# Performance work log

Measured on AMD Instinct MI355X. Metric: run time of the kernel, lower is better.

Reference implementation:

```python
import jax, jax.numpy as jnp
import numpy as np

EPS = 1e-8
THR = 1e-6


def setup_inputs() -> dict:
    key = jax.random.key(0)
    ks = jax.random.split(key, 16)
    B, N, E, F, H, NH = 2, 8192, 131072, 128, 256, 4
    D = H // NH          # per-head width = 64
    FEAT = 2 * F + 12    # 268 = 2F + radial + dist + dot + 9 so3
    s = 0.05
    return {
        "h": jax.random.normal(ks[0], (B, N, F), jnp.float32),
        "coord": jax.random.normal(ks[1], (B, N, 3), jnp.float32),
        "edge_index": jax.random.randint(ks[2], (2, E), 0, N),
        "edge_w1": jax.random.normal(ks[3], (NH, FEAT, D), jnp.float32) * s,
        "edge_b1": jnp.zeros((NH, D), jnp.float32),
        "edge_w2": jax.random.normal(ks[4], (NH, D, D), jnp.float32) * s,
        "edge_b2": jnp.zeros((NH, D), jnp.float32),
        "ln_g": jnp.ones((H,), jnp.float32),
        "ln_b": jnp.zeros((H,), jnp.float32),
        "node_w1": jax.random.normal(ks[5], (H + F, H), jnp.float32) * s,
        "node_b1": jnp.zeros((H,), jnp.float32),
        "node_w2": jax.random.normal(ks[6], (H, F), jnp.float32) * s,
        "node_b2": jnp.zeros((F,), jnp.float32),
        "coord_w1": jax.random.normal(ks[7], (H, H), jnp.float32) * s,
        "coord_b1": jnp.zeros((H,), jnp.float32),
        "coord_w2": jax.random.normal(ks[8], (H, 1), jnp.float32) * 0.001,  # xavier gain 0.001
    }


def reference(h, coord, edge_index, edge_w1, edge_b1, edge_w2, edge_b2,
              ln_g, ln_b, node_w1, node_b1, node_w2, node_b2,
              coord_w1, coord_b1, coord_w2):
    B, N, F = h.shape
    row, col = edge_index[0], edge_index[1]
    ci, ck = coord[:, row], coord[:, col]            # (B,E,3) gathers
    coord_diff = ci - ck
    radial = jnp.sum(coord_diff * coord_diff, axis=-1, keepdims=True)
    dist = jnp.sqrt(radial)
    dot = jnp.sum(ci * ck, axis=-1, keepdims=True)
    # SO3 local frame per edge
    a = coord_diff / (dist + EPS)
    cr = jnp.cross(ci, ck)
    b = cr / (jnp.linalg.norm(cr, axis=-1, keepdims=True) + EPS)
    c = jnp.cross(a, b)
    bad = ((jnp.linalg.norm(a, axis=-1) < THR) |
           (jnp.linalg.norm(b, axis=-1) < THR) |
           (jnp.linalg.norm(c, axis=-1) < THR))
    so3 = jnp.stack([a, b, c], axis=-1)              # (B,E,3,3) columns a,b,c
    eye = jnp.broadcast_to(jnp.eye(3, dtype=so3.dtype), so3.shape)
    so3 = jnp.where(bad[..., None, None], eye, so3).reshape(B, -1, 9)
    # edge features -> multi-head edge MLPs
    feat = jnp.concatenate([h[:, row], h[:, col], radial, dist, dot, so3], axis=-1)  # (B,E,268)
    hmid = jax.nn.silu(jnp.einsum('bef,hfd->bhed', feat, edge_w1) + edge_b1[None, :, None, :])
    heads = jnp.einsum('bhed,hdk->bhek', hmid, edge_w2) + edge_b2[None, :, None, :]
    combined = jnp.moveaxis(heads, 1, 2).reshape(B, heads.shape[2], -1)  # (B,E,H)
    mu = jnp.mean(combined, axis=-1, keepdims=True)
    var = jnp.var(combined, axis=-1, keepdims=True)
    edge_feat = (combined - mu) / jnp.sqrt(var + 1e-5) * ln_g + ln_b
    # coordinate update: scatter-add weighted coord_diff
    w = jax.nn.silu(edge_feat @ coord_w1 + coord_b1) @ coord_w2   # (B,E,1)
    seg = lambda d: jax.ops.segment_sum(d, row, num_segments=N)
    coord_out = coord + jax.vmap(seg)(coord_diff * w)
    # node update: scatter-add edge features then MLP with residual
    agg = jax.vmap(seg)(edge_feat)                                # (B,N,H)
    out = jnp.concatenate([h, agg], axis=-1)
    out = jax.nn.silu(out @ node_w1 + node_b1) @ node_w2 + node_b2
    return h + out, coord_out
```

## Files before the change

### kernel.cpp

```cpp
#include <hip/hip_runtime.h>
#include <hip/hip_bf16.h>
#include <cstdint>
#include <cstddef>

#define BB 2
#define NN 8192
#define EE 131072
#define FFdim 128
#define HHdim 256
#define NHEAD 4
#define DHEAD 64
#define FEATD 268
#define K1PAD 288
#define SF 296
#define SH 264
#define TE 64
#define NT 32
#define SA 392
#define SM 264

typedef short bf16x8 __attribute__((ext_vector_type(8)));
typedef float floatx4 __attribute__((ext_vector_type(4)));

__device__ __forceinline__ float silu_f(float x) {
    return x * __fdividef(1.0f, 1.0f + __expf(-x));
}
__device__ __forceinline__ unsigned short f2bf(float x) {
    unsigned int u = __float_as_uint(x);
    unsigned int r = (u + 0x7fffu + ((u >> 16) & 1u)) >> 16;
    return (unsigned short)r;
}
__device__ __forceinline__ float bf2f(unsigned short u) {
    return __uint_as_float(((unsigned int)u) << 16);
}
__device__ __forceinline__ unsigned int pk2bf(float x, float y) {
    float2 f = { x, y };
    __hip_bfloat162 t = __float22bfloat162_rn(f);
    union { __hip_bfloat162 b; unsigned int u; } cv;
    cv.b = t;
    return cv.u;
}
__device__ __forceinline__ float rowsum16(float v) {
    v += __int_as_float(__builtin_amdgcn_update_dpp(0, __float_as_int(v), 0x128, 0xf, 0xf, true));
    v += __int_as_float(__builtin_amdgcn_update_dpp(0, __float_as_int(v), 0x124, 0xf, 0xf, true));
    v += __int_as_float(__builtin_amdgcn_update_dpp(0, __float_as_int(v), 0x122, 0xf, 0xf, true));
    v += __int_as_float(__builtin_amdgcn_update_dpp(0, __float_as_int(v), 0x121, 0xf, 0xf, true));
    return v;
}
__device__ __forceinline__ int operm(int p) { return ((p & 3) << 4) | (p >> 2); }

#define W1T_ELEMS (256 * K1PAD)
#define W2T_ELEMS (256 * 64)
#define CW1T_ELEMS (256 * 256)
#define NW1T_ELEMS (256 * 384)
#define NW2T_ELEMS (128 * 256)
#define HBF_ELEMS (BB * NN * FFdim)
#define WT_A (W1T_ELEMS)
#define WT_B (W1T_ELEMS + W2T_ELEMS)
#define WT_C (W1T_ELEMS + W2T_ELEMS + CW1T_ELEMS)
#define WT_D (WT_C + NW1T_ELEMS)
#define WT_E (WT_D + NW2T_ELEMS)
#define WT_F (WT_E + NN)
#define WT_G (WT_F + HBF_ELEMS)
__global__ void prep_weights(const float* __restrict__ w1,
                             const float* __restrict__ w2,
                             const float* __restrict__ cw1,
                             const float* __restrict__ nw1,
                             const float* __restrict__ nw2,
                             const float* __restrict__ h,
                             unsigned short* __restrict__ w1T,
                             unsigned short* __restrict__ w2T,
                             unsigned short* __restrict__ cw1T,
                             unsigned short* __restrict__ nw1T,
                             unsigned short* __restrict__ nw2T,
                             unsigned short* __restrict__ hbf,
                             int* __restrict__ counts) {
    int idx = blockIdx.x * blockDim.x + threadIdx.x;
    if (idx < WT_A) {
        int n = idx / K1PAD, k = idx % K1PAD;
        int hh = n >> 6, d = n & 63;
        float v = (k < FEATD) ? w1[((size_t)hh * FEATD + k) * DHEAD + d] : 0.f;
        w1T[idx] = f2bf(v);
    } else if (idx < WT_B) {
        int j = idx - WT_A;
        int n = j >> 6, p = j & 63;
        int hh = n >> 6, dout = n & 63;
        int din = operm(p);
        w2T[j] = f2bf(w2[(size_t)hh * 4096 + din * 64 + dout]);
    } else if (idx < WT_C) {
        int j = idx - WT_B;
        int n = j >> 8, P = j & 255;
        int ko = (P >> 6) * 64 + operm(P & 63);
        cw1T[j] = f2bf(cw1[ko * 256 + n]);
    } else if (idx < WT_D) {
        int j = idx - WT_C;
        int n = j / 384, k = j % 384;
        int ko = (k < 128) ? k : 128 + ((k - 128) >> 6) * 64 + operm(k & 63);
        nw1T[j] = f2bf(nw1[ko * 256 + n]);
    } else if (idx < WT_E) {
        int j = idx - WT_D;
        int n = j >> 8, P = j & 255;
        int ko = (P >> 6) * 64 + operm(P & 63);
        nw2T[j] = f2bf(nw2[ko * 128 + n]);
    } else if (idx < WT_F) {
        counts[idx - WT_E] = 0;
    } else if (idx < WT_G) {
        int j = idx - WT_F;
        hbf[j] = f2bf(h[j]);
    }
}

__global__ void csr_count(const int* __restrict__ eidx, int* __restrict__ counts) {
    int e = blockIdx.x * 256 + threadIdx.x;
    atomicAdd(&counts[eidx[e]], 1);
}

__global__ void csr_scan(const int* __restrict__ counts,
                         int* __restrict__ offsets,
                         int* __restrict__ cursor) {
    __shared__ int wsum[4];
    const int t = threadIdx.x;
    const int base = t * 32;
    int local[32];
    int s = 0;
#pragma unroll
    for (int i = 0; i < 32; ++i) { local[i] = counts[base + i]; s += local[i]; }
    const int lane = t & 63, w = t >> 6;
    int v = s;
#pragma unroll
    for (int off = 1; off < 64; off <<= 1) {
        int u = __shfl_up(v, off, 64);
        if (lane >= off) v += u;
    }
    if (lane == 63) wsum[w] = v;
    __syncthreads();
    int wbase = 0;
    for (int i = 0; i < w; ++i) wbase += wsum[i];
    int run = wbase + v - s;
#pragma unroll
    for (int i = 0; i < 32; ++i) {
        offsets[base + i] = run;
        cursor[base + i] = run;
        run += local[i];
    }
    if (t == 255) offsets[NN] = run;
}

__global__ void csr_fill(const int* __restrict__ eidx,
                         int* __restrict__ cursor, int* __restrict__ perm) {
    int e = blockIdx.x * 256 + threadIdx.x;
    int r = eidx[e];
    int pos = atomicAdd(&cursor[r], 1);
    perm[e] = pos;
}

__global__ __launch_bounds__(256, 4)
void edge_kernel(const unsigned short* __restrict__ hbf,
                 const float* __restrict__ coord,
                 const int* __restrict__ eidx,
                 const int* __restrict__ perm,
                 const unsigned short* __restrict__ w1T, const float* __restrict__ b1,
                 const unsigned short* __restrict__ w2T, const float* __restrict__ b2,
                 const float* __restrict__ lng, const float* __restrict__ lnb,
                 const unsigned short* __restrict__ cw1T, const float* __restrict__ cb1,
                 const float* __restrict__ cw2,
                 unsigned short* __restrict__ efb, float4* __restrict__ wd) {
    __shared__ unsigned short bufA[TE * SF];
    __shared__ int slot_s[TE];
    __shared__ float cd_s[TE][3];
    __shared__ float lns[TE], lns2[TE];
    __shared__ float scr[TE * 4];

    const int tid = threadIdx.x;
    const int b = blockIdx.y;
    const int e0 = blockIdx.x * TE;
    const int lane = tid & 63;
    const int w = tid >> 6;
    const int lm = lane & 15;
    const int quad = lane >> 4;
    const int koff = quad * 8;

    if (tid < TE) {
        lns[tid] = 0.f; lns2[tid] = 0.f;
        const int e = e0 + tid;
        const int r = eidx[e], c = eidx[EE + e];
        slot_s[tid] = perm[e];
        const float* pi = coord + ((size_t)b * NN + r) * 3;
        const float* pk = coord + ((size_t)b * NN + c) * 3;
        float ci0 = pi[0], ci1 = pi[1], ci2 = pi[2];
        float ck0 = pk[0], ck1 = pk[1], ck2 = pk[2];
        float dx = ci0 - ck0, dy = ci1 - ck1, dz = ci2 - ck2;
        float radial = dx * dx + dy * dy + dz * dz;
        float dist = sqrtf(radial);
        float dotv = ci0 * ck0 + ci1 * ck1 + ci2 * ck2;
        float inva = __fdividef(1.0f, dist + 1e-8f);
        float a0 = dx * inva, a1 = dy * inva, a2 = dz * inva;
        float cr0 = ci1 * ck2 - ci2 * ck1;
        float cr1 = ci2 * ck0 - ci0 * ck2;
        float cr2 = ci0 * ck1 - ci1 * ck0;
        float nb = sqrtf(cr0 * cr0 + cr1 * cr1 + cr2 * cr2);
        float invb = __fdividef(1.0f, nb + 1e-8f);
        float b0 = cr0 * invb, b1v = cr1 * invb, b2v = cr2 * invb;
        float c0 = a1 * b2v - a2 * b1v;
        float c1 = a2 * b0 - a0 * b2v;
        float c2 = a0 * b1v - a1 * b0;
        float na = sqrtf(a0 * a0 + a1 * a1 + a2 * a2);
        float nbn = sqrtf(b0 * b0 + b1v * b1v + b2v * b2v);
        float nc = sqrtf(c0 * c0 + c1 * c1 + c2 * c2);
        bool bad = (na < 1e-6f) || (nbn < 1e-6f) || (nc < 1e-6f);
        float s[12];
        s[0] = radial; s[1] = dist; s[2] = dotv;
        if (bad) {
            s[3] = 1.f; s[4] = 0.f; s[5] = 0.f;
            s[6] = 0.f; s[7] = 1.f; s[8] = 0.f;
            s[9] = 0.f; s[10] = 0.f; s[11] = 1.f;
        } else {
            s[3] = a0;  s[4] = b0;  s[5] = c0;
            s[6] = a1;  s[7] = b1v; s[8] = c1;
            s[9] = a2;  s[10] = b2v; s[11] = c2;
        }
        unsigned short* fp = &bufA[tid * SF];
#pragma unroll
        for (int q = 0; q < 12; ++q) fp[256 + q] = f2bf(s[q]);
#pragma unroll
        for (int q = FEATD; q < K1PAD; ++q) fp[q] = 0;
        cd_s[tid][0] = dx; cd_s[tid][1] = dy; cd_s[tid][2] = dz;
    }
    for (int idx = tid; idx < TE * 32; idx += 256) {
        const int e = idx >> 5, c16 = idx & 31;
        const int node = (c16 < 16) ? eidx[e0 + e] : eidx[EE + e0 + e];
        const int cc = (c16 & 15) * 8;
        uint4 v = *(const uint4*)&hbf[((size_t)b * NN + node) * FFdim + cc];
        *(uint4*)&bufA[e * SF + c16 * 8] = v;
    }
    __syncthreads();

    floatx4 acc[4][4];
#pragma unroll
    for (int i = 0; i < 4; ++i)
#pragma unroll
        for (int j = 0; j < 4; ++j)
#pragma unroll
            for (int q = 0; q < 4; ++q) acc[i][j][q] = 0.f;
#pragma unroll
    for (int ks = 0; ks < K1PAD / 32; ++ks) {
        const int kb = ks * 32 + koff;
        bf16x8 a[4], bfr[4];
#pragma unroll
        for (int rt = 0; rt < 4; ++rt)
            a[rt] = *(const bf16x8*)&bufA[(rt * 16 + lm) * SF + kb];
#pragma unroll
        for (int ct = 0; ct < 4; ++ct)
            bfr[ct] = *(const bf16x8*)&w1T[(size_t)(w * 64 + ct * 16 + lm) * K1PAD + kb];
#pragma unroll
        for (int rt = 0; rt < 4; ++rt)
#pragma unroll
            for (int ct = 0; ct < 4; ++ct)
                acc[rt][ct] = __builtin_amdgcn_mfma_f32_16x16x32_bf16(
                    a[rt], bfr[ct], acc[rt][ct], 0, 0, 0);
    }
    float bias1[4];
#pragma unroll
    for (int ct = 0; ct < 4; ++ct) bias1[ct] = b1[w * 64 + ct * 16 + lm];
    __syncthreads();
#pragma unroll
    for (int rt = 0; rt < 4; ++rt)
#pragma unroll
        for (int reg = 0; reg < 4; ++reg) {
            const int row = rt * 16 + quad * 4 + reg;
            uint2 pk;
            pk.x = pk2bf(silu_f(acc[rt][0][reg] + bias1[0]),
                         silu_f(acc[rt][1][reg] + bias1[1]));
            pk.y = pk2bf(silu_f(acc[rt][2][reg] + bias1[2]),
                         silu_f(acc[rt][3][reg] + bias1[3]));
            *(uint2*)&bufA[row * SH + w * 64 + lm * 4] = pk;
        }

    floatx4 acc2[4][4];
#pragma unroll
    for (int i = 0; i < 4; ++i)
#pragma unroll
        for (int j = 0; j < 4; ++j)
#pragma unroll
            for (int q = 0; q < 4; ++q) acc2[i][j][q] = 0.f;
#pragma unroll
    for (int ks = 0; ks < 2; ++ks) {
        const int kb = ks * 32 + koff;
        bf16x8 a[4], bfr[4];
#pragma unroll
        for (int rt = 0; rt < 4; ++rt)
            a[rt] = *(const bf16x8*)&bufA[(rt * 16 + lm) * SH + w * 64 + kb];
#pragma unroll
        for (int ct = 0; ct < 4; ++ct)
            bfr[ct] = *(const bf16x8*)&w2T[(size_t)(w * 64 + ct * 16 + lm) * 64 + kb];
#pragma unroll
        for (int rt = 0; rt < 4; ++rt)
#pragma unroll
            for (int ct = 0; ct < 4; ++ct)
                acc2[rt][ct] = __builtin_amdgcn_mfma_f32_16x16x32_bf16(
                    a[rt], bfr[ct], acc2[rt][ct], 0, 0, 0);
    }
    float bias2[4];
#pragma unroll
    for (int ct = 0; ct < 4; ++ct) bias2[ct] = b2[w * 64 + ct * 16 + lm];
#pragma unroll
    for (int rt = 0; rt < 4; ++rt)
#pragma unroll
        for (int reg = 0; reg < 4; ++reg) {
            float s = 0.f, s2 = 0.f;
#pragma unroll
            for (int ct = 0; ct < 4; ++ct) {
                float v = acc2[rt][ct][reg] + bias2[ct];
                acc2[rt][ct][reg] = v;
                s += v; s2 += v * v;
            }
            s = rowsum16(s);
            s2 = rowsum16(s2);
            if (lm == 0) {
                const int row = rt * 16 + quad * 4 + reg;
                atomicAdd(&lns[row], s);
                atomicAdd(&lns2[row], s2);
            }
        }
    __syncthreads();
    if (tid < TE) {
        float mean = lns[tid] * (1.0f / 256.0f);
        float var = lns2[tid] * (1.0f / 256.0f) - mean * mean;
        scr[tid] = mean;
        scr[TE + tid] = rsqrtf(var + 1e-5f);
    }
    __syncthreads();
    {
        float gv[4], bv[4];
#pragma unroll
        for (int ct = 0; ct < 4; ++ct) {
            const int col = w * 64 + ct * 16 + lm;
            gv[ct] = lng[col]; bv[ct] = lnb[col];
        }
#pragma unroll
        for (int rt = 0; rt < 4; ++rt)
#pragma unroll
            for (int reg = 0; reg < 4; ++reg) {
                const int row = rt * 16 + quad * 4 + reg;
                const float mu = scr[row], rs = scr[TE + row];
                uint2 pk;
                pk.x = pk2bf((acc2[rt][0][reg] - mu) * rs * gv[0] + bv[0],
                             (acc2[rt][1][reg] - mu) * rs * gv[1] + bv[1]);
                pk.y = pk2bf((acc2[rt][2][reg] - mu) * rs * gv[2] + bv[2],
                             (acc2[rt][3][reg] - mu) * rs * gv[3] + bv[3]);
                *(uint2*)&bufA[row * SH + w * 64 + lm * 4] = pk;
            }
    }
    __syncthreads();

    floatx4 acc3[4][4];
#pragma unroll
    for (int i = 0; i < 4; ++i)
#pragma unroll
        for (int j = 0; j < 4; ++j)
#pragma unroll
            for (int q = 0; q < 4; ++q) acc3[i][j][q] = 0.f;
#pragma unroll
    for (int ks = 0; ks < 8; ++ks) {
        const int kb = ks * 32 + koff;
        bf16x8 a[4], bfr[4];
#pragma unroll
        for (int rt = 0; rt < 4; ++rt)
            a[rt] = *(const bf16x8*)&bufA[(rt * 16 + lm) * SH + kb];
#pragma unroll
        for (int ct = 0; ct < 4; ++ct)
            bfr[ct] = *(const bf16x8*)&cw1T[(size_t)(w * 64 + ct * 16 + lm) * 256 + kb];
#pragma unroll
        for (int rt = 0; rt < 4; ++rt)
#pragma unroll
            for (int ct = 0; ct < 4; ++ct)
                acc3[rt][ct] = __builtin_amdgcn_mfma_f32_16x16x32_bf16(
                    a[rt], bfr[ct], acc3[rt][ct], 0, 0, 0);
    }
    {
        float cb[4], cwv[4];
#pragma unroll
        for (int ct = 0; ct < 4; ++ct) {
            const int col = w * 64 + ct * 16 + lm;
            cb[ct] = cb1[col]; cwv[ct] = cw2[col];
        }
#pragma unroll
        for (int rt = 0; rt < 4; ++rt)
#pragma unroll
            for (int reg = 0; reg < 4; ++reg) {
                float s = 0.f;
#pragma unroll
                for (int ct = 0; ct < 4; ++ct)
                    s += silu_f(acc3[rt][ct][reg] + cb[ct]) * cwv[ct];
                s = rowsum16(s);
                if (lm == 0) scr[(rt * 16 + quad * 4 + reg) * 4 + w] = s;
            }
    }
    __syncthreads();

    if (tid < TE) {
        float ww = scr[tid * 4] + scr[tid * 4 + 1] + scr[tid * 4 + 2] + scr[tid * 4 + 3];
        float4 o = { cd_s[tid][0] * ww, cd_s[tid][1] * ww, cd_s[tid][2] * ww, 0.f };
        wd[(size_t)b * EE + slot_s[tid]] = o;
    }
    for (int idx = tid; idx < TE * 32; idx += 256) {
        const int e = idx >> 5, c = idx & 31;
        uint4 v = *(const uint4*)&bufA[e * SH + c * 8];
        *(uint4*)&efb[((size_t)b * EE + slot_s[e]) * HHdim + c * 8] = v;
    }
}

__global__ __launch_bounds__(256, 4)
void node_kernel(const float* __restrict__ h,
                 const unsigned short* __restrict__ hbf,
                 const float* __restrict__ coord,
                 const unsigned short* __restrict__ efb,
                 const float4* __restrict__ wd,
                 const int* __restrict__ offsets,
                 const unsigned short* __restrict__ nw1T, const float* __restrict__ nb1,
                 const unsigned short* __restrict__ nw2T, const float* __restrict__ nb2,
                 float* __restrict__ hout, float* __restrict__ coord_out) {
    __shared__ unsigned short bufN[NT * SA];

    const int tid = threadIdx.x;
    const int b = blockIdx.y;
    const int n0 = blockIdx.x * NT;
    const int lane = tid & 63;
    const int w = tid >> 6;
    const int lm = lane & 15;
    const int quad = lane >> 4;
    const int koff = quad * 8;

    for (int idx = tid; idx < NT * 16; idx += 256) {
        const int r = idx >> 4, c8 = idx & 15;
        uint4 v = *(const uint4*)&hbf[((size_t)b * NN + n0 + r) * FFdim + c8 * 8];
        *(uint4*)&bufN[r * SA + c8 * 8] = v;
    }

    for (int i = 0; i < 8; ++i) {
        const int r = w * 8 + i;
        const int n = n0 + r;
        const int o0 = offsets[n], o1 = offsets[n + 1];
        float a0 = 0.f, a1 = 0.f, a2 = 0.f, a3 = 0.f;
        const unsigned short* ebase = efb + (size_t)b * EE * HHdim + lane * 4;
        int j = o0;
        for (; j + 4 <= o1; j += 4) {
            ushort4 u0 = *(const ushort4*)(ebase + (size_t)(j + 0) * HHdim);
            ushort4 u1 = *(const ushort4*)(ebase + (size_t)(j + 1) * HHdim);
            ushort4 u2 = *(const ushort4*)(ebase + (size_t)(j + 2) * HHdim);
            ushort4 u3 = *(const ushort4*)(ebase + (size_t)(j + 3) * HHdim);
            a0 += bf2f(u0.x) + bf2f(u1.x) + bf2f(u2.x) + bf2f(u3.x);
            a1 += bf2f(u0.y) + bf2f(u1.y) + bf2f(u2.y) + bf2f(u3.y);
            a2 += bf2f(u0.z) + bf2f(u1.z) + bf2f(u2.z) + bf2f(u3.z);
            a3 += bf2f(u0.w) + bf2f(u1.w) + bf2f(u2.w) + bf2f(u3.w);
        }
        for (; j < o1; ++j) {
            ushort4 u = *(const ushort4*)(ebase + (size_t)j * HHdim);
            a0 += bf2f(u.x); a1 += bf2f(u.y); a2 += bf2f(u.z); a3 += bf2f(u.w);
        }
        uint2 pk;
        pk.x = pk2bf(a0, a1);
        pk.y = pk2bf(a2, a3);
        *(uint2*)&bufN[r * SA + FFdim + lane * 4] = pk;

        float sx = 0.f, sy = 0.f, sz = 0.f;
        for (int jj = o0 + lane; jj < o1; jj += 64) {
            float4 t = wd[(size_t)b * EE + jj];
            sx += t.x; sy += t.y; sz += t.z;
        }
#pragma unroll
        for (int m = 1; m < 64; m <<= 1) {
            sx += __shfl_xor(sx, m, 64);
            sy += __shfl_xor(sy, m, 64);
            sz += __shfl_xor(sz, m, 64);
        }
        if (lane < 3) {
            const size_t cb = ((size_t)b * NN + n) * 3 + lane;
            float s = (lane == 0) ? sx : (lane == 1) ? sy : sz;
            coord_out[cb] = coord[cb] + s;
        }
    }
    __syncthreads();

    floatx4 acc[2][4];
#pragma unroll
    for (int i = 0; i < 2; ++i)
#pragma unroll
        for (int j = 0; j < 4; ++j)
#pragma unroll
            for (int q = 0; q < 4; ++q) acc[i][j][q] = 0.f;
#pragma unroll
    for (int ks = 0; ks < 12; ++ks) {
        const int kb = ks * 32 + koff;
        bf16x8 a[2], bfr[4];
#pragma unroll
        for (int rt = 0; rt < 2; ++rt)
            a[rt] = *(const bf16x8*)&bufN[(rt * 16 + lm) * SA + kb];
#pragma unroll
        for (int ct = 0; ct < 4; ++ct)
            bfr[ct] = *(const bf16x8*)&nw1T[(size_t)(w * 64 + ct * 16 + lm) * 384 + kb];
#pragma unroll
        for (int rt = 0; rt < 2; ++rt)
#pragma unroll
            for (int ct = 0; ct < 4; ++ct)
                acc[rt][ct] = __builtin_amdgcn_mfma_f32_16x16x32_bf16(
                    a[rt], bfr[ct], acc[rt][ct], 0, 0, 0);
    }
    float nb1v[4];
#pragma unroll
    for (int ct = 0; ct < 4; ++ct) nb1v[ct] = nb1[w * 64 + ct * 16 + lm];
    __syncthreads();
#pragma unroll
    for (int rt = 0; rt < 2; ++rt)
#pragma unroll
        for (int reg = 0; reg < 4; ++reg) {
            const int row = rt * 16 + quad * 4 + reg;
            uint2 pk;
            pk.x = pk2bf(silu_f(acc[rt][0][reg] + nb1v[0]),
                         silu_f(acc[rt][1][reg] + nb1v[1]));
            pk.y = pk2bf(silu_f(acc[rt][2][reg] + nb1v[2]),
                         silu_f(acc[rt][3][reg] + nb1v[3]));
            *(uint2*)&bufN[row * SM + w * 64 + lm * 4] = pk;
        }
    __syncthreads();

    floatx4 accb[2][2];
#pragma unroll
    for (int i = 0; i < 2; ++i)
#pragma unroll
        for (int j = 0; j < 2; ++j)
#pragma unroll
            for (int q = 0; q < 4; ++q) accb[i][j][q] = 0.f;
#pragma unroll
    for (int ks = 0; ks < 8; ++ks) {
        const int kb = ks * 32 + koff;
        bf16x8 a[2], bfr[2];
#pragma unroll
        for (int rt = 0; rt < 2; ++rt)
            a[rt] = *(const bf16x8*)&bufN[(rt * 16 + lm) * SM + kb];
#pragma unroll
        for (int ct = 0; ct < 2; ++ct)
            bfr[ct] = *(const bf16x8*)&nw2T[(size_t)(w * 32 + ct * 16 + lm) * 256 + kb];
#pragma unroll
        for (int rt = 0; rt < 2; ++rt)
#pragma unroll
            for (int ct = 0; ct < 2; ++ct)
                accb[rt][ct] = __builtin_amdgcn_mfma_f32_16x16x32_bf16(
                    a[rt], bfr[ct], accb[rt][ct], 0, 0, 0);
    }
#pragma unroll
    for (int ct = 0; ct < 2; ++ct) {
        const int col = w * 32 + ct * 16 + lm;
        const float bias = nb2[col];
#pragma unroll
        for (int rt = 0; rt < 2; ++rt)
#pragma unroll
            for (int reg = 0; reg < 4; ++reg) {
                const int row = rt * 16 + quad * 4 + reg;
                const size_t gi = ((size_t)b * NN + n0 + row) * FFdim + col;
                hout[gi] = accb[rt][ct][reg] + bias + h[gi];
            }
    }
}

extern "C" void kernel_launch(void* const* d_in, const int* in_sizes, int n_in,
                              void* d_out, int out_size, void* d_ws, size_t ws_size,
                              hipStream_t stream) {
    const float* h     = (const float*)d_in[0];
    const float* coord = (const float*)d_in[1];
    const int*   eidx  = (const int*)d_in[2];
    const float* w1    = (const float*)d_in[3];
    const float* b1    = (const float*)d_in[4];
    const float* w2    = (const float*)d_in[5];
    const float* b2    = (const float*)d_in[6];
    const float* lng   = (const float*)d_in[7];
    const float* lnb   = (const float*)d_in[8];
    const float* nw1   = (const float*)d_in[9];
    const float* nb1   = (const float*)d_in[10];
    const float* nw2   = (const float*)d_in[11];
    const float* nb2   = (const float*)d_in[12];
    const float* cw1   = (const float*)d_in[13];
    const float* cb1   = (const float*)d_in[14];
    const float* cw2   = (const float*)d_in[15];

    float* hout = (float*)d_out;
    float* coord_out = hout + (size_t)BB * NN * FFdim;

    char* p = (char*)d_ws;
    float4* wd = (float4*)p;                   p += (size_t)BB * EE * 16;
    unsigned short* efb = (unsigned short*)p;  p += (size_t)BB * EE * HHdim * 2;
    unsigned short* hbf = (unsigned short*)p;  p += (size_t)HBF_ELEMS * 2;
    unsigned short* w1T = (unsigned short*)p;  p += (size_t)W1T_ELEMS * 2;
    unsigned short* w2T = (unsigned short*)p;  p += (size_t)W2T_ELEMS * 2;
    unsigned short* cw1T = (unsigned short*)p; p += (size_t)CW1T_ELEMS * 2;
    unsigned short* nw1T = (unsigned short*)p; p += (size_t)NW1T_ELEMS * 2;
    unsigned short* nw2T = (unsigned short*)p; p += (size_t)NW2T_ELEMS * 2;
    int* counts = (int*)p;                     p += (size_t)NN * 4;
    int* offsets = (int*)p;                    p += (size_t)(NN + 1) * 4;
    int* cursor = (int*)p;                     p += (size_t)NN * 4;
    int* perm = (int*)p;                       p += (size_t)EE * 4;

    hipLaunchKernelGGL(prep_weights, dim3((WT_G + 255) / 256), dim3(256),
                       0, stream, w1, w2, cw1, nw1, nw2, h,
                       w1T, w2T, cw1T, nw1T, nw2T, hbf, counts);
    hipLaunchKernelGGL(csr_count, dim3(EE / 256), dim3(256), 0, stream, eidx, counts);
    hipLaunchKernelGGL(csr_scan, dim3(1), dim3(256), 0, stream, counts, offsets, cursor);
    hipLaunchKernelGGL(csr_fill, dim3(EE / 256), dim3(256), 0, stream, eidx, cursor, perm);
    hipLaunchKernelGGL(edge_kernel, dim3(EE / TE, BB), dim3(256), 0, stream,
                       hbf, coord, eidx, perm, w1T, b1, w2T, b2, lng, lnb, cw1T, cb1, cw2,
                       efb, wd);
    hipLaunchKernelGGL(node_kernel, dim3(NN / NT, BB), dim3(256), 0, stream,
                       h, hbf, coord, efb, wd, offsets, nw1T, nb1, nw2T, nb2,
                       hout, coord_out);
}
```

Baseline: 343.8 us.

## Fuse CSR slot assignment into edge kernel and widen node aggregation loads

Removes the separate csr_fill kernel and its perm buffer. Each edge now claims its CSR slot with an atomicAdd on a per-batch cursor inside the edge kernel, which saves one launch and one pass over the edge indices but adds atomics to the edge kernel. The scan vectorises its count loads, and the node aggregation now reads 16-byte rows with two half-waves processing alternate edges, merged by a shuffle. Slot order within a segment becomes nondeterministic, which can change the floating-point summation order.

```diff
diff --git a/kernel.cpp b/kernel.cpp
--- a/kernel.cpp
+++ b/kernel.cpp
@@ -122,9 +122,15 @@
     const int t = threadIdx.x;
     const int base = t * 32;
     int local[32];
+#pragma unroll
+    for (int q = 0; q < 8; ++q) {
+        uint4 c4 = ((const uint4*)counts)[t * 8 + q];
+        local[q * 4 + 0] = c4.x; local[q * 4 + 1] = c4.y;
+        local[q * 4 + 2] = c4.z; local[q * 4 + 3] = c4.w;
+    }
     int s = 0;
 #pragma unroll
-    for (int i = 0; i < 32; ++i) { local[i] = counts[base + i]; s += local[i]; }
+    for (int i = 0; i < 32; ++i) s += local[i];
     const int lane = t & 63, w = t >> 6;
     int v = s;
 #pragma unroll
@@ -141,24 +147,17 @@
     for (int i = 0; i < 32; ++i) {
         offsets[base + i] = run;
         cursor[base + i] = run;
+        cursor[NN + base + i] = run;
         run += local[i];
     }
     if (t == 255) offsets[NN] = run;
-}
-
-__global__ void csr_fill(const int* __restrict__ eidx,
-                         int* __restrict__ cursor, int* __restrict__ perm) {
-    int e = blockIdx.x * 256 + threadIdx.x;
-    int r = eidx[e];
-    int pos = atomicAdd(&cursor[r], 1);
-    perm[e] = pos;
 }
 
 __global__ __launch_bounds__(256, 4)
 void edge_kernel(const unsigned short* __restrict__ hbf,
                  const float* __restrict__ coord,
                  const int* __restrict__ eidx,
-                 const int* __restrict__ perm,
+                 int* __restrict__ cursor,
                  const unsigned short* __restrict__ w1T, const float* __restrict__ b1,
                  const unsigned short* __restrict__ w2T, const float* __restrict__ b2,
                  const float* __restrict__ lng, const float* __restrict__ lnb,
@@ -184,7 +183,7 @@
         lns[tid] = 0.f; lns2[tid] = 0.f;
         const int e = e0 + tid;
         const int r = eidx[e], c = eidx[EE + e];
-        slot_s[tid] = perm[e];
+        slot_s[tid] = atomicAdd(&cursor[b * NN + r], 1);
         const float* pi = coord + ((size_t)b * NN + r) * 3;
         const float* pk = coord + ((size_t)b * NN + c) * 3;
         float ci0 = pi[0], ci1 = pi[1], ci2 = pi[2];
@@ -430,6 +429,8 @@
     const int lm = lane & 15;
     const int quad = lane >> 4;
     const int koff = quad * 8;
+    const int half = lane >> 5;
+    const int cl = lane & 31;
 
     for (int idx = tid; idx < NT * 16; idx += 256) {
         const int r = idx >> 4, c8 = idx & 15;
@@ -441,27 +442,29 @@
         const int r = w * 8 + i;
         const int n = n0 + r;
         const int o0 = offsets[n], o1 = offsets[n + 1];
-        float a0 = 0.f, a1 = 0.f, a2 = 0.f, a3 = 0.f;
-        const unsigned short* ebase = efb + (size_t)b * EE * HHdim + lane * 4;
-        int j = o0;
-        for (; j + 4 <= o1; j += 4) {
-            ushort4 u0 = *(const ushort4*)(ebase + (size_t)(j + 0) * HHdim);
-            ushort4 u1 = *(const ushort4*)(ebase + (size_t)(j + 1) * HHdim);
-            ushort4 u2 = *(const ushort4*)(ebase + (size_t)(j + 2) * HHdim);
-            ushort4 u3 = *(const ushort4*)(ebase + (size_t)(j + 3) * HHdim);
-            a0 += bf2f(u0.x) + bf2f(u1.x) + bf2f(u2.x) + bf2f(u3.x);
-            a1 += bf2f(u0.y) + bf2f(u1.y) + bf2f(u2.y) + bf2f(u3.y);
-            a2 += bf2f(u0.z) + bf2f(u1.z) + bf2f(u2.z) + bf2f(u3.z);
-            a3 += bf2f(u0.w) + bf2f(u1.w) + bf2f(u2.w) + bf2f(u3.w);
-        }
-        for (; j < o1; ++j) {
-            ushort4 u = *(const ushort4*)(ebase + (size_t)j * HHdim);
-            a0 += bf2f(u.x); a1 += bf2f(u.y); a2 += bf2f(u.z); a3 += bf2f(u.w);
-        }
-        uint2 pk;
-        pk.x = pk2bf(a0, a1);
-        pk.y = pk2bf(a2, a3);
-        *(uint2*)&bufN[r * SA + FFdim + lane * 4] = pk;
+        float f[8];
+#pragma unroll
+        for (int q = 0; q < 8; ++q) f[q] = 0.f;
+        const unsigned short* ebase = efb + (size_t)b * EE * HHdim + cl * 8;
+        for (int j = o0 + half; j < o1; j += 2) {
+            uint4 u = *(const uint4*)(ebase + (size_t)j * HHdim);
+            f[0] += bf2f((unsigned short)(u.x & 0xffff));
+            f[1] += bf2f((unsigned short)(u.x >> 16));
+            f[2] += bf2f((unsigned short)(u.y & 0xffff));
+            f[3] += bf2f((unsigned short)(u.y >> 16));
+            f[4] += bf2f((unsigned short)(u.z & 0xffff));
+            f[5] += bf2f((unsigned short)(u.z >> 16));
+            f[6] += bf2f((unsigned short)(u.w & 0xffff));
+            f[7] += bf2f((unsigned short)(u.w >> 16));
+        }
+#pragma unroll
+        for (int q = 0; q < 8; ++q) f[q] += __shfl_xor(f[q], 32, 64);
+        if (half == 0) {
+            uint4 pk;
+            pk.x = pk2bf(f[0], f[1]); pk.y = pk2bf(f[2], f[3]);
+            pk.z = pk2bf(f[4], f[5]); pk.w = pk2bf(f[6], f[7]);
+            *(uint4*)&bufN[r * SA + FFdim + cl * 8] = pk;
+        }
 
         float sx = 0.f, sy = 0.f, sz = 0.f;
         for (int jj = o0 + lane; jj < o1; jj += 64) {
@@ -597,18 +600,16 @@
     unsigned short* nw2T = (unsigned short*)p; p += (size_t)NW2T_ELEMS * 2;
     int* counts = (int*)p;                     p += (size_t)NN * 4;
     int* offsets = (int*)p;                    p += (size_t)(NN + 1) * 4;
-    int* cursor = (int*)p;                     p += (size_t)NN * 4;
-    int* perm = (int*)p;                       p += (size_t)EE * 4;
+    int* cursor = (int*)p;                     p += (size_t)2 * NN * 4;
 
     hipLaunchKernelGGL(prep_weights, dim3((WT_G + 255) / 256), dim3(256),
                        0, stream, w1, w2, cw1, nw1, nw2, h,
                        w1T, w2T, cw1T, nw1T, nw2T, hbf, counts);
     hipLaunchKernelGGL(csr_count, dim3(EE / 256), dim3(256), 0, stream, eidx, counts);
     hipLaunchKernelGGL(csr_scan, dim3(1), dim3(256), 0, stream, counts, offsets, cursor);
-    hipLaunchKernelGGL(csr_fill, dim3(EE / 256), dim3(256), 0, stream, eidx, cursor, perm);
     hipLaunchKernelGGL(edge_kernel, dim3(EE / TE, BB), dim3(256), 0, stream,
-                       hbf, coord, eidx, perm, w1T, b1, w2T, b2, lng, lnb, cw1T, cb1, cw2,
-                       efb, wd);
+                       hbf, coord, eidx, cursor, w1T, b1, w2T, b2, lng, lnb,
+                       cw1T, cb1, cw2, efb, wd);
     hipLaunchKernelGGL(node_kernel, dim3(NN / NT, BB), dim3(256), 0, stream,
                        h, hbf, coord, efb, wd, offsets, nw1T, nb1, nw2T, nb2,
                        hout, coord_out);
```

After: 350.0 us. About the same (+1.8%).
